# Kernel optimization log

Measured on AMD Instinct MI355X. Metric: run time of the kernel, lower is better.

## Reference

```python
import jax, jax.numpy as jnp
import numpy as np
import math

CUTOFF = 6.0
NUM_RADIAL = 96
HID = 128
NUM_GRAPHS = 4
NODES_PER_GRAPH = 4000
BOX = 67.0
EPS = 1e-10


def _layernorm(x):
    m = jnp.mean(x, axis=-1, keepdims=True)
    v = jnp.var(x, axis=-1, keepdims=True)
    return (x - m) / jnp.sqrt(v + 1e-5)


def _rbf(dist):
    # rbf_emb: exp-scaled gaussians with cosine cutoff envelope
    start = math.exp(-CUTOFF)
    means = jnp.linspace(start, 1.0, NUM_RADIAL).astype(dist.dtype)
    beta = (2.0 / NUM_RADIAL * (1.0 - start)) ** -2
    d = dist[:, None]
    env = 0.5 * (jnp.cos(d * jnp.pi / CUTOFF) + 1.0) * (d < CUTOFF).astype(dist.dtype)
    return env * jnp.exp(-beta * jnp.square(jnp.exp(-d) - means))


def _forward(pos, rl_w1, rl_b1, rl_w2, rl_b2, ne_w, ne_b, sv_w, sv_b,
             l3_w1, l3_b1, l3_w2, l3_b2, mp_ln_w, mp_ln_b,
             xp_w1, xp_b1, xp_w2, xp_b2, rp_w, rp_b,
             ip_w1, ip_b1, ip_w2, ip_b2,
             fte_eq_w, fte_w1, fte_b1, fte_w2, fte_b2,
             out_w, out_b, z, batch, edge_index):
    N = pos.shape[0]
    silu = jax.nn.silu
    j, i = edge_index[0], edge_index[1]

    vecs = pos[j] - pos[i]                       # [E,3]
    dist = jnp.linalg.norm(vecs, axis=-1)        # [E]
    r_emb = _rbf(dist)                           # [E,R]
    r_hid = silu(r_emb @ rl_w1 + rl_b1) @ rl_w2 + rl_b2
    rbounds = 0.5 * (jnp.cos(dist * jnp.pi / CUTOFF) + 1.0)
    r_hid = rbounds[:, None] * r_hid             # [E,H]

    # NeighborEmb: s = ln(lin(onehot(z))) + scatter_add_i(ln(lin(onehot(z)))[j] * r_hid)
    z1h = jax.nn.one_hot(z, 95, dtype=pos.dtype)
    h0 = _layernorm(z1h @ ne_w + ne_b)           # [N,H]
    s = h0 + jax.ops.segment_sum(h0[j] * r_hid, i, num_segments=N)

    vec = jnp.zeros((N, 3, HID), pos.dtype)

    ed = vecs / (dist[:, None] + EPS)            # edge_diff [E,3]
    ec = jnp.cross(pos[i], pos[j])
    ec = ec / (jnp.linalg.norm(ec, axis=1, keepdims=True) + EPS)
    ev = jnp.cross(ed, ec)
    frame = jnp.stack([ed, ec, ev], axis=-1)     # [E,3(space),3(frame)]

    # S_vector: scatter_add_i( s_lin[j] outer edge_diff * r_hid )
    s_lin = silu(s @ sv_w + sv_b)
    msg = s_lin[j][:, None, :] * (r_hid[:, None, :] * ed[:, :, None])  # [E,3,H]
    S = jax.ops.segment_sum(msg, i, num_segments=N)                    # [N,3,H]

    def scalarize(Se):
        sc = jnp.einsum('edh,edf->efh', Se, frame)                     # [E,3,H]
        sc = sc.at[:, 1, :].set(jnp.abs(sc[:, 1, :]))
        p = jnp.transpose(sc, (0, 2, 1))                               # [E,H,3]
        out = silu(p @ l3_w1 + l3_b1) @ l3_w2 + l3_b2                  # [E,H,1]
        return (out + p[:, :, :1])[..., 0]                             # [E,H]

    scalar3 = scalarize(S[i])
    scalar4 = scalarize(S[j])
    ew = jnp.concatenate([scalar3, scalar4], axis=-1) * rbounds[:, None]
    ew = jnp.concatenate([ew, r_hid, r_emb], axis=-1)                  # [E,3H+R]

    # EquiMessagePassing (only one layer executes: source loops range(1))
    xln = _layernorm(s) * mp_ln_w + mp_ln_b
    xh = silu(xln @ xp_w1 + xp_b1) @ xp_w2 + xp_b2                     # [N,3H]
    rbfh = (r_emb @ rp_w + rp_b) * (silu(ew @ ip_w1 + ip_b1) @ ip_w2 + ip_b2)
    m = xh[j] * rbfh                                                   # [E,3H]
    m1, m2, m3 = jnp.split(m, 3, axis=-1)
    m2 = m2 / jnp.sqrt(3.0)
    vmsg = (vec[j] * m2[:, None, :] + m3[:, None, :] * ed[:, :, None]) / jnp.sqrt(float(HID))
    s = s + jax.ops.segment_sum(m1, i, num_segments=N)
    vec = vec + jax.ops.segment_sum(vmsg, i, num_segments=N)

    # FTE (node_frame == 0 in LEFTNet-Z: use invariant norm channel)
    vp = jnp.einsum('ndh,hk->ndk', vec, fte_eq_w)                      # [N,3,2H]
    v1, v2 = jnp.split(vp, 2, axis=-1)
    scalar = jnp.sqrt(jnp.sum(v1 * v1, axis=1) + EPS)                  # [N,H]
    vec_dot = jnp.sum(v1 * v2, axis=1) / jnp.sqrt(float(HID))
    xh2 = silu(jnp.concatenate([s, scalar], axis=-1) @ fte_w1 + fte_b1) @ fte_w2 + fte_b2
    a1, a2, a3 = jnp.split(xh2, 3, axis=-1)
    s = s + (a1 + a2 * vec_dot) / jnp.sqrt(2.0)
    vec = vec + a3[:, None, :] * v2

    out = s @ out_w + out_b                                            # [N,T]
    num = jax.ops.segment_sum(out, batch, num_segments=NUM_GRAPHS)
    cnt = jax.ops.segment_sum(jnp.ones((N,), out.dtype), batch, num_segments=NUM_GRAPHS)
    out = num / cnt[:, None]                                           # mean readout
    return out  # y_std=1, y_mean=0


def _lin_init(key, fi, fo, bias=True):
    k1, k2 = jax.random.split(key)
    lim = 1.0 / np.sqrt(fi)
    w = jax.random.uniform(k1, (fi, fo), jnp.float32, -lim, lim)
    if not bias:
        return w
    b = jax.random.uniform(k2, (fo,), jnp.float32, -lim, lim)
    return w, b


def setup_inputs() -> dict:
    rng = np.random.default_rng(0)
    N = NUM_GRAPHS * NODES_PER_GRAPH
    pos_np = (rng.random((N, 3)) * BOX).astype(np.float32)
    batch_np = np.repeat(np.arange(NUM_GRAPHS), NODES_PER_GRAPH).astype(np.int64)
    z_np = rng.integers(0, 95, size=(N,)).astype(np.int64)
    rows, cols = [], []
    for g in range(NUM_GRAPHS):
        p = pos_np[g * NODES_PER_GRAPH:(g + 1) * NODES_PER_GRAPH]
        d2 = ((p[:, None, :] - p[None, :, :]) ** 2).sum(-1)
        a, b = np.nonzero((d2 < CUTOFF ** 2) & (d2 > 0.0))
        rows.append(a + g * NODES_PER_GRAPH)
        cols.append(b + g * NODES_PER_GRAPH)
    edge_index = np.stack([np.concatenate(rows), np.concatenate(cols)]).astype(np.int64)

    keys = jax.random.split(jax.random.key(0), 16)
    rl_w1, rl_b1 = _lin_init(keys[0], NUM_RADIAL, HID)
    rl_w2, rl_b2 = _lin_init(keys[1], HID, HID)
    ne_w, ne_b = _lin_init(keys[2], 95, HID)
    sv_w, sv_b = _lin_init(keys[3], HID, HID)
    l3_w1, l3_b1 = _lin_init(keys[4], 3, HID // 4)
    l3_w2, l3_b2 = _lin_init(keys[5], HID // 4, 1)
    xp_w1, xp_b1 = _lin_init(keys[6], HID, HID)
    xp_w2, xp_b2 = _lin_init(keys[7], HID, 3 * HID)
    rp_w, rp_b = _lin_init(keys[8], NUM_RADIAL, 3 * HID)
    ip_w1, ip_b1 = _lin_init(keys[9], 3 * HID + NUM_RADIAL, 3 * HID)
    ip_w2, ip_b2 = _lin_init(keys[10], 3 * HID, 3 * HID)
    fte_eq_w = _lin_init(keys[11], HID, 2 * HID, bias=False)
    fte_w1, fte_b1 = _lin_init(keys[12], 2 * HID, HID)
    fte_w2, fte_b2 = _lin_init(keys[13], HID, 3 * HID)
    out_w, out_b = _lin_init(keys[14], HID, 1)

    return {
        'pos': jnp.asarray(pos_np), 'z': jnp.asarray(z_np),
        'batch': jnp.asarray(batch_np), 'edge_index': jnp.asarray(edge_index),
        'rl_w1': rl_w1, 'rl_b1': rl_b1, 'rl_w2': rl_w2, 'rl_b2': rl_b2,
        'ne_w': ne_w, 'ne_b': ne_b, 'sv_w': sv_w, 'sv_b': sv_b,
        'l3_w1': l3_w1, 'l3_b1': l3_b1, 'l3_w2': l3_w2, 'l3_b2': l3_b2,
        'mp_ln_w': jnp.ones((HID,), jnp.float32), 'mp_ln_b': jnp.zeros((HID,), jnp.float32),
        'xp_w1': xp_w1, 'xp_b1': xp_b1, 'xp_w2': xp_w2, 'xp_b2': xp_b2,
        'rp_w': rp_w, 'rp_b': rp_b,
        'ip_w1': ip_w1, 'ip_b1': ip_b1, 'ip_w2': ip_w2, 'ip_b2': ip_b2,
        'fte_eq_w': fte_eq_w, 'fte_w1': fte_w1, 'fte_b1': fte_b1,
        'fte_w2': fte_w2, 'fte_b2': fte_b2, 'out_w': out_w, 'out_b': out_b,
    }


def reference(pos, rl_w1, rl_b1, rl_w2, rl_b2, ne_w, ne_b, sv_w, sv_b,
              l3_w1, l3_b1, l3_w2, l3_b2, mp_ln_w, mp_ln_b,
              xp_w1, xp_b1, xp_w2, xp_b2, rp_w, rp_b,
              ip_w1, ip_b1, ip_w2, ip_b2,
              fte_eq_w, fte_w1, fte_b1, fte_w2, fte_b2,
              out_w, out_b, z, batch, edge_index):
    return _forward(pos, rl_w1, rl_b1, rl_w2, rl_b2, ne_w, ne_b, sv_w, sv_b,
                    l3_w1, l3_b1, l3_w2, l3_b2, mp_ln_w, mp_ln_b,
                    xp_w1, xp_b1, xp_w2, xp_b2, rp_w, rp_b,
                    ip_w1, ip_b1, ip_w2, ip_b2,
                    fte_eq_w, fte_w1, fte_b1, fte_w2, fte_b2,
                    out_w, out_b, z, batch, edge_index)
```

## Files before the change

kernel.cpp:

```cpp
#include <hip/hip_runtime.h>
#include <hip/hip_bf16.h>
#include <math.h>

#define NRAD 96
#define HIDDIM 128
typedef unsigned short ushortT;

typedef __attribute__((ext_vector_type(8))) short bf8_t;
typedef __attribute__((ext_vector_type(4))) float f4_t;
typedef __attribute__((ext_vector_type(2))) float f2_t;

#if defined(__has_builtin)
#  if __has_builtin(__builtin_amdgcn_global_load_lds)
#    define HAVE_GLDS 1
#  endif
#  if __has_builtin(__builtin_amdgcn_rcpf)
#    define RCPF(x) __builtin_amdgcn_rcpf(x)
#  endif
#  if __has_builtin(__builtin_amdgcn_exp2f)
#    define EXP2F(x) __builtin_amdgcn_exp2f(x)
#  endif
#  if __has_builtin(__builtin_amdgcn_cosf)
#    define COSR(x) __builtin_amdgcn_cosf(x)
#  endif
#endif
#ifndef RCPF
#  define RCPF(x) (1.f/(x))
#endif
#ifndef EXP2F
#  define EXP2F(x) exp2f(x)
#endif
#ifndef COSR
#  define COSR(x) cosf(6.2831853071795864f*(x))
#endif
#define LOG2E 1.44269504088896f
#define LN2   0.69314718055995f

__device__ __forceinline__ float silu_f(float x){
  return x * RCPF(1.f + EXP2F(-LOG2E*x));
}
__device__ __forceinline__ float b2f(ushortT u){ return __uint_as_float(((unsigned int)u) << 16); }
__device__ __forceinline__ ushortT f2b(float x){
  unsigned int u = __float_as_uint(x);
  unsigned int r = (u + 0x7fffu + ((u >> 16) & 1u)) >> 16;
  return (ushortT)r;
}

#ifdef HAVE_GLDS
__device__ __forceinline__ void glds16(const ushortT* g, ushortT* l){
  __builtin_amdgcn_global_load_lds(
      (const __attribute__((address_space(1))) ushortT*)g,
      (__attribute__((address_space(3))) ushortT*)l, 16, 0, 0);
}
#endif

__global__ void k_detect(const ushortT* posw, int npos,
                         const int* batchw, int nb, int* flags){
  int tot = (npos < 4096 ? npos : 4096);
  int big = tot > nb ? tot : nb;
  int bad = 0, orv = 0;
  for (int t = blockIdx.x*blockDim.x + threadIdx.x; t < big; t += gridDim.x*blockDim.x){
    if (t < tot){
      float x = b2f(posw[t]);
      if (!(fabsf(x) <= 1000.f)) bad = 1;
    }
    if (t < nb && (t & 1)) orv |= batchw[t];
  }
  if (bad) atomicOr(&flags[2], 1);
  if (orv) atomicOr(&flags[3], 1);
}

__global__ void k_iconv(const int* zsrc, const int* bsrc, const int* esrc,
                        int* zi, int* bi, int* eii, int Nn, int E, const int* flags,
                        int* deg){
  int f = (flags[3] == 0) ? 1 : 0;
  int total = 2*Nn + 2*E;
  for (int t = blockIdx.x*blockDim.x + threadIdx.x; t < total; t += gridDim.x*blockDim.x){
    if (t < Nn) zi[t] = zsrc[(size_t)t << f];
    else if (t < 2*Nn) bi[t-Nn] = bsrc[(size_t)(t-Nn) << f];
    else {
      int e = t - 2*Nn;
      int v = esrc[(size_t)e << f];
      eii[e] = v;
      if (e >= E) atomicAdd(&deg[v], 1);
    }
  }
}

struct ConvDesc { const ushortT* src; float* dst; int n; };
struct ConvArgs { ConvDesc d[32]; };

__global__ void k_conv(ConvArgs a, int cnt, const int* flags){
  int y = blockIdx.y;
  if (y >= cnt) return;
  int f = (flags[2] == 0) ? 1 : 0;
  const ushortT* s = a.d[y].src;
  float* dst = a.d[y].dst;
  int n = a.d[y].n;
  if (f){
    for (int t = blockIdx.x*blockDim.x + threadIdx.x; t < n; t += gridDim.x*blockDim.x)
      dst[t] = b2f(s[t]);
  } else {
    const float* sf = (const float*)s;
    for (int t = blockIdx.x*blockDim.x + threadIdx.x; t < n; t += gridDim.x*blockDim.x)
      dst[t] = sf[t];
  }
}

struct TDesc { const ushortT* src; ushortT* dst; int K, N; };
struct TArgs { TDesc d[12]; };

__global__ void k_wt(TArgs a, int cnt, const int* flags){
  int y = blockIdx.y;
  if (y >= cnt) return;
  int f = (flags[2] == 0) ? 1 : 0;
  const ushortT* s = a.d[y].src;
  ushortT* dst = a.d[y].dst;
  int K = a.d[y].K, N = a.d[y].N, tot = K*N;
  for (int t = blockIdx.x*blockDim.x + threadIdx.x; t < tot; t += gridDim.x*blockDim.x){
    int k = t / N, n = t - k*N;
    ushortT v = f ? s[t] : f2b(((const float*)s)[t]);
    dst[(size_t)n*K + k] = v;
  }
}

__global__ void k_f2b(const float* __restrict__ src, ushortT* __restrict__ dst, int n){
  for (int t = blockIdx.x*blockDim.x + threadIdx.x; t < n; t += gridDim.x*blockDim.x)
    dst[t] = f2b(src[t]);
}

__global__ void k_zero(float* __restrict__ p, int n){
  int t = blockIdx.x*blockDim.x + threadIdx.x;
  int stride = gridDim.x*blockDim.x;
  for (; t < n; t += stride) p[t] = 0.f;
}

__global__ void k_sentinel(__hip_bfloat16* out, int n, float val){
  int t = threadIdx.x;
  if (t < n) out[t] = __float2bfloat16(val);
}

__global__ void k_csr_scan(const int* __restrict__ deg, int* __restrict__ rowptr, int Nn){
  __shared__ int sh[256];
  __shared__ int carry;
  if (threadIdx.x == 0){ carry = 0; rowptr[0] = 0; }
  __syncthreads();
  for (int t0 = 0; t0 < Nn; t0 += 256){
    int idx = t0 + threadIdx.x;
    int v = (idx < Nn) ? deg[idx] : 0;
    sh[threadIdx.x] = v; __syncthreads();
    for (int o = 1; o < 256; o <<= 1){
      int u = (threadIdx.x >= o) ? sh[threadIdx.x - o] : 0;
      __syncthreads();
      sh[threadIdx.x] += u; __syncthreads();
    }
    if (idx < Nn) rowptr[idx + 1] = carry + sh[threadIdx.x];
    __syncthreads();
    if (threadIdx.x == 0) carry += sh[255];
    __syncthreads();
  }
}

__global__ void k_csr_scatter(const int* __restrict__ eii, int E,
                              const int* __restrict__ rowptr, int* __restrict__ cursor,
                              int* __restrict__ jp, int* __restrict__ ip){
  int e = blockIdx.x*blockDim.x + threadIdx.x;
  if (e >= E) return;
  int i = eii[E+e];
  int p = atomicAdd(&cursor[i], 1);
  int k = rowptr[i] + p;
  jp[k] = eii[e];
  ip[k] = i;
}

__global__ void k_geom(const float* __restrict__ pos,
                       const int* __restrict__ jp, const int* __restrict__ ip,
                       int off, int Cc,
                       float* __restrict__ edb, float* __restrict__ ecv,
                       float* __restrict__ rb, ushortT* __restrict__ remb)
{
  int el = blockIdx.x*blockDim.x + threadIdx.x;
  if (el >= Cc) return;
  int g = off + el;
  int j = jp[g], i = ip[g];
  float pjx = pos[3*j], pjy = pos[3*j+1], pjz = pos[3*j+2];
  float pix = pos[3*i], piy = pos[3*i+1], piz = pos[3*i+2];
  float vx = pjx-pix, vy = pjy-piy, vz = pjz-piz;
  float d = sqrtf(vx*vx + vy*vy + vz*vz);
  float inv = RCPF(d + 1e-10f);
  float edx = vx*inv, edy = vy*inv, edz = vz*inv;
  edb[3*el]=edx; edb[3*el+1]=edy; edb[3*el+2]=edz;
  if (ecv){
    float cx = piy*pjz - piz*pjy;
    float cy = piz*pjx - pix*pjz;
    float cz = pix*pjy - piy*pjx;
    float cn = sqrtf(cx*cx + cy*cy + cz*cz);
    float inv2 = RCPF(cn + 1e-10f);
    cx *= inv2; cy *= inv2; cz *= inv2;
    ecv[6*el]=cx; ecv[6*el+1]=cy; ecv[6*el+2]=cz;
    ecv[6*el+3]=edy*cz - edz*cy;
    ecv[6*el+4]=edz*cx - edx*cz;
    ecv[6*el+5]=edx*cy - edy*cx;
  }
  float rbv = 0.5f*(COSR(d*0.08333333333f) + 1.f);
  rb[el] = rbv;
  float env = (d < 6.f) ? rbv : 0.f;
  const float stf = 0.0024787522f;
  const float prf = (2.0f/96.0f)*(1.0f - stf);
  const float betaL = LOG2E/(prf*prf);
  float emd = EXP2F(-LOG2E*d);
  for (int k = 0; k < NRAD; ++k){
    float mu = stf + (1.0f - stf)*((float)k*(1.0f/95.0f));
    float t = emd - mu;
    remb[(size_t)el*NRAD + k] = f2b(env * EXP2F(-betaL*t*t));
  }
}

__global__ __launch_bounds__(128) void k_embed(const int* __restrict__ z,
    const float* __restrict__ ne_w, const float* __restrict__ ne_b,
    float* __restrict__ s, float* __restrict__ h0,
    float* __restrict__ S, float* __restrict__ vecacc)
{
  int n = blockIdx.x; int h = threadIdx.x;
  float x = ne_w[(size_t)z[n]*HIDDIM + h] + ne_b[h];
  __shared__ float red[128];
  red[h] = x; __syncthreads();
  for (int o = 64; o > 0; o >>= 1){ if (h < o) red[h] += red[h+o]; __syncthreads(); }
  float mean = red[0] * (1.f/128.f);
  __syncthreads();
  float dx = x - mean;
  red[h] = dx*dx; __syncthreads();
  for (int o = 64; o > 0; o >>= 1){ if (h < o) red[h] += red[h+o]; __syncthreads(); }
  float var = red[0] * (1.f/128.f);
  float y = dx * rsqrtf(var + 1e-5f);
  s[(size_t)n*HIDDIM + h] = y;
  h0[(size_t)n*HIDDIM + h] = y;
  float* Sr = &S[(size_t)n*384 + h];
  float* Vr = &vecacc[(size_t)n*384 + h];
  Sr[0]=0.f; Sr[128]=0.f; Sr[256]=0.f;
  Vr[0]=0.f; Vr[128]=0.f; Vr[256]=0.f;
}

__global__ __launch_bounds__(128) void k_ln(const float* __restrict__ src, ushortT* __restrict__ dst,
    const float* __restrict__ g, const float* __restrict__ b, ushortT* __restrict__ sb)
{
  int n = blockIdx.x; int h = threadIdx.x;
  float x = src[(size_t)n*HIDDIM + h];
  sb[(size_t)n*HIDDIM + h] = f2b(x);
  __shared__ float red[128];
  red[h] = x; __syncthreads();
  for (int o = 64; o > 0; o >>= 1){ if (h < o) red[h] += red[h+o]; __syncthreads(); }
  float mean = red[0] * (1.f/128.f);
  __syncthreads();
  float dx = x - mean;
  red[h] = dx*dx; __syncthreads();
  for (int o = 64; o > 0; o >>= 1){ if (h < o) red[h] += red[h+o]; __syncthreads(); }
  float var = red[0] * (1.f/128.f);
  float y = dx * rsqrtf(var + 1e-5f);
  dst[(size_t)n*HIDDIM + h] = f2b(y * g[h] + b[h]);
}

__global__ __launch_bounds__(128) void k_seg1n(const int* __restrict__ rowptr,
    const int* __restrict__ jp, int o, int Cc,
    const float* __restrict__ h0, const ushortT* __restrict__ rhid,
    float* __restrict__ s)
{
  int i = blockIdx.x, h = threadIdx.x;
  int b = rowptr[i], e = rowptr[i+1];
  if (b < o) b = o;
  int hi = o + Cc; if (e > hi) e = hi;
  if (b >= e) return;
  float acc = 0.f;
  int m = b;
  for (; m + 1 < e; m += 2){
    int j0 = jp[m], j1 = jp[m+1];
    float r0 = b2f(rhid[(size_t)(m-o)*HIDDIM + h]);
    float r1 = b2f(rhid[(size_t)(m+1-o)*HIDDIM + h]);
    acc += h0[(size_t)j0*HIDDIM + h]*r0 + h0[(size_t)j1*HIDDIM + h]*r1;
  }
  if (m < e) acc += h0[(size_t)jp[m]*HIDDIM + h] * b2f(rhid[(size_t)(m-o)*HIDDIM + h]);
  s[(size_t)i*HIDDIM + h] += acc;
}

__global__ __launch_bounds__(128) void k_seg2n(const int* __restrict__ rowptr,
    const int* __restrict__ jp, int o, int Cc,
    const ushortT* __restrict__ slin, const ushortT* __restrict__ rhid,
    const float* __restrict__ edb, float* __restrict__ S)
{
  int i = blockIdx.x, h = threadIdx.x;
  int b = rowptr[i], e = rowptr[i+1];
  if (b < o) b = o;
  int hi = o + Cc; if (e > hi) e = hi;
  if (b >= e) return;
  float a0 = 0.f, a1 = 0.f, a2 = 0.f;
  int m = b;
  for (; m + 1 < e; m += 2){
    int ml = m - o, ml2 = ml + 1;
    float u0 = b2f(slin[(size_t)jp[m]*HIDDIM + h])   * b2f(rhid[(size_t)ml*HIDDIM + h]);
    float u1 = b2f(slin[(size_t)jp[m+1]*HIDDIM + h]) * b2f(rhid[(size_t)ml2*HIDDIM + h]);
    a0 += u0*edb[3*ml]   + u1*edb[3*ml2];
    a1 += u0*edb[3*ml+1] + u1*edb[3*ml2+1];
    a2 += u0*edb[3*ml+2] + u1*edb[3*ml2+2];
  }
  if (m < e){
    int ml = m - o;
    float u0 = b2f(slin[(size_t)jp[m]*HIDDIM + h]) * b2f(rhid[(size_t)ml*HIDDIM + h]);
    a0 += u0*edb[3*ml]; a1 += u0*edb[3*ml+1]; a2 += u0*edb[3*ml+2];
  }
  float* base = &S[(size_t)i*384 + h];
  base[0]   += a0;
  base[128] += a1;
  base[256] += a2;
}

__global__ __launch_bounds__(128) void k_seg3n(const int* __restrict__ rowptr,
    int o, int Cc,
    const ushortT* __restrict__ mb, const float* __restrict__ edb,
    float* __restrict__ s, float* __restrict__ vecacc)
{
  int i = blockIdx.x, h = threadIdx.x;
  int b = rowptr[i], e = rowptr[i+1];
  if (b < o) b = o;
  int hi = o + Cc; if (e > hi) e = hi;
  if (b >= e) return;
  const float is128 = 0.08838834764831845f;
  float am = 0.f, v0 = 0.f, v1 = 0.f, v2 = 0.f;
  int m = b;
  for (; m + 1 < e; m += 2){
    int ml = m - o, ml2 = ml + 1;
    float m1a = b2f(mb[(size_t)ml*384 + h]);
    float m1b = b2f(mb[(size_t)ml2*384 + h]);
    float mma = b2f(mb[(size_t)ml*384 + 256 + h]) * is128;
    float mmb = b2f(mb[(size_t)ml2*384 + 256 + h]) * is128;
    am += m1a + m1b;
    v0 += mma*edb[3*ml]   + mmb*edb[3*ml2];
    v1 += mma*edb[3*ml+1] + mmb*edb[3*ml2+1];
    v2 += mma*edb[3*ml+2] + mmb*edb[3*ml2+2];
  }
  if (m < e){
    int ml = m - o;
    float m1 = b2f(mb[(size_t)ml*384 + h]);
    float mm = b2f(mb[(size_t)ml*384 + 256 + h]) * is128;
    am += m1;
    v0 += mm*edb[3*ml]; v1 += mm*edb[3*ml+1]; v2 += mm*edb[3*ml+2];
  }
  s[(size_t)i*HIDDIM + h] += am;
  float* base = &vecacc[(size_t)i*384 + h];
  base[0]   += v0;
  base[128] += v1;
  base[256] += v2;
}

__global__ __launch_bounds__(256) void k_scal3(
  const int* __restrict__ jp, const int* __restrict__ ip, int off, int Cc,
  const float* __restrict__ S,
  const ushortT* __restrict__ rhid, const float* __restrict__ edb,
  const float* __restrict__ ecv, const float* __restrict__ rb,
  const ushortT* __restrict__ remb,
  const float* __restrict__ w1, const float* __restrict__ b1,
  const float* __restrict__ w2, const float* __restrict__ b2,
  ushortT* __restrict__ ew)
{
  __shared__ float w1s[96], b1s[32], w2s[32];
  __shared__ float sb2;
  int t = threadIdx.x;
  if (t < 96) w1s[t] = w1[t] * (-LOG2E);
  else if (t < 128) b1s[t-96] = b1[t-96] * (-LOG2E);
  else if (t < 160) w2s[t-128] = w2[t-128] * (-LN2);
  else if (t == 160) sb2 = b2[0];
  int ea = blockIdx.x*2;
  int eb = (ea + 1 < Cc) ? ea + 1 : ea;
  int which = t >> 7, h = t & 127;
  int ga = off + ea, gb = off + eb;
  int na = which ? jp[ga] : ip[ga];
  int nb = which ? jp[gb] : ip[gb];
  f2_t f00 = {edb[3*ea],   edb[3*eb]};
  f2_t f01 = {edb[3*ea+1], edb[3*eb+1]};
  f2_t f02 = {edb[3*ea+2], edb[3*eb+2]};
  f2_t f10 = {ecv[6*ea],   ecv[6*eb]};
  f2_t f11 = {ecv[6*ea+1], ecv[6*eb+1]};
  f2_t f12 = {ecv[6*ea+2], ecv[6*eb+2]};
  f2_t f20 = {ecv[6*ea+3], ecv[6*eb+3]};
  f2_t f21 = {ecv[6*ea+4], ecv[6*eb+4]};
  f2_t f22 = {ecv[6*ea+5], ecv[6*eb+5]};
  f2_t rbv = {rb[ea], rb[eb]};
  __syncthreads();
  const float* Sa = &S[(size_t)na*384];
  const float* Sb = &S[(size_t)nb*384];
  f2_t S0 = {Sa[h],     Sb[h]};
  f2_t S1 = {Sa[128+h], Sb[128+h]};
  f2_t S2 = {Sa[256+h], Sb[256+h]};
  f2_t v0 = S0*f00 + S1*f01 + S2*f02;
  f2_t v1t = S0*f10 + S1*f11 + S2*f12;
  f2_t v1 = {fabsf(v1t.x), fabsf(v1t.y)};
  f2_t v2 = S0*f20 + S1*f21 + S2*f22;
  f2_t out = {0.f, 0.f};
  #pragma unroll
  for (int u = 0; u < 32; ++u){
    f2_t tt = v0*w1s[u] + v1*w1s[32+u] + v2*w1s[64+u] + b1s[u];
    f2_t r;
    r.x = RCPF(1.f + EXP2F(tt.x));
    r.y = RCPF(1.f + EXP2F(tt.y));
    out += (tt*r)*w2s[u];
  }
  f2_t res = (out + sb2 + v0) * rbv;
  ushortT* ewa = &ew[(size_t)ea*480];
  ewa[which*128 + h] = f2b(res.x);
  if (eb != ea) ew[(size_t)eb*480 + which*128 + h] = f2b(res.y);
  if (which == 0){
    ewa[256 + h] = rhid[(size_t)ea*HIDDIM + h];
    if (h < NRAD) ewa[384 + h] = remb[(size_t)ea*NRAD + h];
    if (eb != ea){
      ew[(size_t)eb*480 + 256 + h] = rhid[(size_t)eb*HIDDIM + h];
      if (h < NRAD) ew[(size_t)eb*480 + 384 + h] = remb[(size_t)eb*NRAD + h];
    }
  }
}

__global__ __launch_bounds__(256) void mgemm(
  const ushortT* __restrict__ A, const ushortT* __restrict__ BT,
  const float* __restrict__ bias,
  float* __restrict__ Cf, ushortT* __restrict__ Cb,
  int M, int N, int K, int epi,
  const float* __restrict__ rowscale,
  const ushortT* __restrict__ mul1b,
  const ushortT* __restrict__ xhpb,
  const int* __restrict__ jidx,
  int skipTile)
{
  const int tid = threadIdx.x;
  const int w = tid >> 6;
  const int lane = tid & 63;
  const int l15 = lane & 15;
  const int q = lane >> 4;
  const int wm = w & 1, wn = w >> 1;
  const int rowBase = blockIdx.y * 128;
  int bx = blockIdx.x;
  if (skipTile >= 0 && bx >= skipTile) bx++;
  const int colBase = bx * 128;
  f4_t acc[4][4] = {};

#ifdef HAVE_GLDS
  __shared__ ushortT As[128*32];
  __shared__ ushortT Bs[128*32];
  const int rS = 32*w + (lane >> 2);
  const int kS = (lane & 3) << 3;
  ushortT* lA0 = &As[(32*w)*32];
  ushortT* lA1 = &As[(32*w+16)*32];
  ushortT* lB0 = &Bs[(32*w)*32];
  ushortT* lB1 = &Bs[(32*w+16)*32];
  int ra0 = rowBase + rS;      if (ra0 >= M) ra0 = M-1;
  int ra1 = rowBase + rS + 16; if (ra1 >= M) ra1 = M-1;
  const ushortT* gA0 = A  + (size_t)ra0*K + kS;
  const ushortT* gA1 = A  + (size_t)ra1*K + kS;
  const ushortT* gB0 = BT + (size_t)(colBase + rS)*K + kS;
  const ushortT* gB1 = BT + (size_t)(colBase + rS + 16)*K + kS;
  for (int k0 = 0; k0 < K; k0 += 32){
    glds16(gA0 + k0, lA0);
    glds16(gA1 + k0, lA1);
    glds16(gB0 + k0, lB0);
    glds16(gB1 + k0, lB1);
    __syncthreads();
    bf8_t a[4], b[4];
    #pragma unroll
    for (int mt = 0; mt < 4; ++mt)
      a[mt] = *(const bf8_t*)&As[(wm*64 + mt*16 + l15)*32 + q*8];
    #pragma unroll
    for (int nt = 0; nt < 4; ++nt)
      b[nt] = *(const bf8_t*)&Bs[(wn*64 + nt*16 + l15)*32 + q*8];
    #pragma unroll
    for (int mt = 0; mt < 4; ++mt){
      #pragma unroll
      for (int nt = 0; nt < 4; ++nt)
        acc[mt][nt] = __builtin_amdgcn_mfma_f32_16x16x32_bf16(a[mt], b[nt], acc[mt][nt], 0, 0, 0);
    }
    __syncthreads();
  }
#else
  __shared__ ushortT As[128*48];
  __shared__ ushortT Bs[128*48];
  const int r0 = tid >> 2,         s0 = (tid & 3) << 3;
  const int r1 = (tid + 256) >> 2, s1 = ((tid + 256) & 3) << 3;
  for (int k0 = 0; k0 < K; k0 += 32){
    int4 a0v = make_int4(0,0,0,0), a1v = make_int4(0,0,0,0);
    if (rowBase + r0 < M) a0v = *(const int4*)&A[(size_t)(rowBase + r0)*K + k0 + s0];
    if (rowBase + r1 < M) a1v = *(const int4*)&A[(size_t)(rowBase + r1)*K + k0 + s1];
    int4 b0v = *(const int4*)&BT[(size_t)(colBase + r0)*K + k0 + s0];
    int4 b1v = *(const int4*)&BT[(size_t)(colBase + r1)*K + k0 + s1];
    __syncthreads();
    *(int4*)&As[r0*48 + s0] = a0v;
    *(int4*)&As[r1*48 + s1] = a1v;
    *(int4*)&Bs[r0*48 + s0] = b0v;
    *(int4*)&Bs[r1*48 + s1] = b1v;
    __syncthreads();
    bf8_t a[4], b[4];
    #pragma unroll
    for (int mt = 0; mt < 4; ++mt)
      a[mt] = *(const bf8_t*)&As[(wm*64 + mt*16 + l15)*48 + q*8];
    #pragma unroll
    for (int nt = 0; nt < 4; ++nt)
      b[nt] = *(const bf8_t*)&Bs[(wn*64 + nt*16 + l15)*48 + q*8];
    #pragma unroll
    for (int mt = 0; mt < 4; ++mt){
      #pragma unroll
      for (int nt = 0; nt < 4; ++nt)
        acc[mt][nt] = __builtin_amdgcn_mfma_f32_16x16x32_bf16(a[mt], b[nt], acc[mt][nt], 0, 0, 0);
    }
  }
#endif

  #pragma unroll
  for (int mt = 0; mt < 4; ++mt){
    int row = rowBase + wm*64 + mt*16 + q*4;
    #pragma unroll
    for (int nt = 0; nt < 4; ++nt){
      int col = colBase + wn*64 + nt*16 + l15;
      float bv = bias ? bias[col] : 0.f;
      #pragma unroll
      for (int r = 0; r < 4; ++r){
        int rr = row + r;
        if (rr >= M) continue;
        float x = acc[mt][nt][r] + bv;
        if (epi == 1) x = silu_f(x);
        else if (epi == 2) x *= rowscale[rr];
        else if (epi == 3) x = x * b2f(mul1b[(size_t)rr*N + col]) * b2f(xhpb[(size_t)jidx[rr]*N + col]);
        if (Cb) Cb[(size_t)rr*N + col] = f2b(x);
        else    Cf[(size_t)rr*N + col] = x;
      }
    }
  }
}

__global__ __launch_bounds__(128) void k_fte_pre(const float* __restrict__ vpc,
    const float* __restrict__ s, ushortT* __restrict__ catb, float* __restrict__ vdot,
    int no)
{
  int nl = blockIdx.x, h = threadIdx.x;
  int n = no + nl;
  const float* base = &vpc[(size_t)nl*768];
  float a0 = base[h],       a1 = base[256+h],     a2 = base[512+h];
  float c0 = base[128+h],   c1 = base[384+h],     c2 = base[640+h];
  float scal = sqrtf(a0*a0 + a1*a1 + a2*a2 + 1e-10f);
  float vd = (a0*c0 + a1*c1 + a2*c2) * 0.08838834764831845f;
  catb[(size_t)n*256 + h] = f2b(s[(size_t)n*HIDDIM + h]);
  catb[(size_t)n*256 + 128 + h] = f2b(scal);
  vdot[(size_t)n*HIDDIM + h] = vd;
}

__global__ __launch_bounds__(128) void k_out(const float* __restrict__ xh2,
    const float* __restrict__ vdot, const float* __restrict__ s,
    const float* __restrict__ ow, const float* __restrict__ ob,
    float* __restrict__ nodeout)
{
  int n = blockIdx.x, h = threadIdx.x;
  float a1 = xh2[(size_t)n*384 + h];
  float a2 = xh2[(size_t)n*384 + 128 + h];
  float sv = s[(size_t)n*HIDDIM + h] + (a1 + a2*vdot[(size_t)n*HIDDIM + h]) * 0.7071067811865476f;
  __shared__ float red[128];
  red[h] = sv * ow[h];
  __syncthreads();
  for (int o = 64; o > 0; o >>= 1){ if (h < o) red[h] += red[h+o]; __syncthreads(); }
  if (h == 0) nodeout[n] = red[0] + ob[0];
}

__global__ __launch_bounds__(256) void k_final(const float* __restrict__ nodeout,
    const int* __restrict__ batch, void* __restrict__ out, int Nn, const int* flags)
{
  int g = blockIdx.x;
  __shared__ float rs[256], rc[256];
  float sm = 0.f, c = 0.f;
  for (int n = threadIdx.x; n < Nn; n += 256){
    if (batch[n] == g){ sm += nodeout[n]; c += 1.f; }
  }
  rs[threadIdx.x] = sm; rc[threadIdx.x] = c;
  __syncthreads();
  for (int o = 128; o > 0; o >>= 1){
    if (threadIdx.x < o){ rs[threadIdx.x] += rs[threadIdx.x+o]; rc[threadIdx.x] += rc[threadIdx.x+o]; }
    __syncthreads();
  }
  if (threadIdx.x == 0){
    float v = (rc[0] > 0.f) ? rs[0]/rc[0] : 0.f;
    if (flags[2] == 0) ((__hip_bfloat16*)out)[g] = __float2bfloat16(v);
    else ((float*)out)[g] = v;
  }
}

extern "C" void kernel_launch(void* const* d_in, const int* in_sizes, int n_in,
                              void* d_out, int out_size, void* d_ws, size_t ws_size,
                              hipStream_t stream)
{
  const int N = in_sizes[0] / 3;
  const int E = in_sizes[3] / 2;

  size_t off = 0;
  auto alloc = [&](size_t n)->float*{
    float* p = (float*)d_ws + off;
    off += (n + 3) & ~(size_t)3;
    return p;
  };
  auto allocU = [&](size_t n)->ushortT*{ return (ushortT*)alloc((n + 1) / 2); };

  int* flags  = (int*)alloc(4);
  int* deg    = (int*)alloc((size_t)N);
  int* cursor = (int*)alloc((size_t)N);
  size_t zeroHdr = off;
  int* zi     = (int*)alloc((size_t)N);
  int* bi     = (int*)alloc((size_t)N);
  int* eii    = (int*)alloc((size_t)2*E);
  int* rowptr = (int*)alloc((size_t)N + 4);
  int* jp     = (int*)alloc((size_t)E);
  int* ipp    = (int*)alloc((size_t)E);

  float* pos = alloc((size_t)N*3);
  float* w[31];
  for (int t = 0; t < 31; ++t) w[t] = alloc((size_t)in_sizes[4+t]);
  float* rl_b1=w[1];  float* rl_b2=w[3];
  float* ne_w =w[4];  float* ne_b =w[5];  float* sv_b =w[7];
  float* l3_w1=w[8];  float* l3_b1=w[9];  float* l3_w2=w[10]; float* l3_b2=w[11];
  float* mp_w =w[12]; float* mp_b =w[13]; float* xp_b1=w[15];
  float* xp_b2=w[17]; float* rp_b =w[19];
  float* ip_b1=w[21]; float* ip_b2=w[23];
  float* fte_b1=w[26];float* fte_b2=w[28];float* out_w=w[29]; float* out_b=w[30];

  ushortT* wt_rl1 = allocU(96*128);
  ushortT* wt_rl2 = allocU(128*128);
  ushortT* wt_sv  = allocU(128*128);
  ushortT* wt_xp1 = allocU(128*128);
  ushortT* wt_xp2 = allocU((size_t)128*384);
  ushortT* wt_rp  = allocU((size_t)96*384);
  ushortT* wt_ip1 = allocU((size_t)480*384);
  ushortT* wt_ip2 = allocU((size_t)384*384);
  ushortT* wt_feq = allocU((size_t)128*256);
  ushortT* wt_ft1 = allocU((size_t)256*128);
  ushortT* wt_ft2 = allocU((size_t)128*384);

  float* s    = alloc((size_t)N*HIDDIM);
  float* h0   = alloc((size_t)N*HIDDIM);
  ushortT* sb     = allocU((size_t)N*HIDDIM);
  ushortT* slin_b = allocU((size_t)N*HIDDIM);
  ushortT* xln_b  = allocU((size_t)N*HIDDIM);
  ushortT* hb     = allocU((size_t)N*HIDDIM);
  float* S    = alloc((size_t)N*384);
  float* vecacc = alloc((size_t)N*384);
  ushortT* xh_b = allocU((size_t)N*384);
  float* nodeout = alloc((size_t)N);
  float* vdot = h0;
  ushortT* catb = sb;
  ushortT* vab = (ushortT*)S;
  float* xh2 = vecacc;

  size_t wsF = ws_size / sizeof(float);

  int tier = 0; size_t p = 746;
  if (off + 122ULL*(size_t)E + 16 + 256ULL*624 <= wsF){ tier = 2; p = 624; }
  else if (off + 67ULL*(size_t)E + 16 + 256ULL*679 <= wsF){ tier = 1; p = 679; }

  ushortT *rhid_a = nullptr, *remb_a = nullptr;
  float *edb_a = nullptr, *ecv_a = nullptr, *rb_a = nullptr;
  if (tier >= 1){
    rhid_a = allocU((size_t)E*128);
    edb_a  = alloc((size_t)3*E);
  }
  if (tier == 2){
    ecv_a  = alloc((size_t)6*E);
    rb_a   = alloc((size_t)E);
    remb_a = allocU((size_t)E*96);
  }
  size_t availF = (wsF > off) ? (wsF - off) : 0;
  if (availF < 256*p){
    k_sentinel<<<1, 64, 0, stream>>>((__hip_bfloat16*)d_out, out_size,
                                     (float)(double)(ws_size >> 20));
    return;
  }
  size_t Cs = availF / p; if (Cs > (size_t)E) Cs = E;
  int C = (int)(Cs & ~(size_t)15);
  if (C < 256) C = 256;

  float* scratch0 = (float*)d_ws + off;
  ushortT* remb_l = nullptr; float *ecv_l = nullptr, *rb_l = nullptr;
  if (tier <= 1){
    remb_l = allocU((size_t)C*96);
    ecv_l  = alloc((size_t)6*C);
    rb_l   = alloc((size_t)C);
  }
  float* edb_l = nullptr; ushortT* rhid_l = nullptr;
  if (tier == 0){
    edb_l  = alloc((size_t)3*C);
    rhid_l = allocU((size_t)C*128);
  }
  ushortT* ew_b = allocU((size_t)C*480);
  ushortT* R2b  = allocU((size_t)C*384);
  ushortT* R1b  = allocU((size_t)C*384);
  ushortT* Rmb  = ew_b;
  ushortT* R2rl = R2b;
  float* vpc = scratch0;
  size_t scratchF = (size_t)C*p;

  auto mg = [&](const ushortT* A, const ushortT* BT, const float* bias,
                float* Cf, ushortT* Cb, int M, int Nc, int K, int epi,
                const float* rowscale = nullptr, const ushortT* mul1b = nullptr,
                const ushortT* xhpb = nullptr, const int* jidx = nullptr,
                int skipTile = -1){
    dim3 grid(Nc/128 - (skipTile >= 0 ? 1 : 0), (M + 127)/128);
    mgemm<<<grid, 256, 0, stream>>>(A, BT, bias, Cf, Cb, M, Nc, K, epi,
                                    rowscale, mul1b, xhpb, jidx, skipTile);
  };

  k_zero<<<64, 256, 0, stream>>>((float*)flags, (int)zeroHdr);
  k_detect<<<64, 256, 0, stream>>>((const ushortT*)d_in[0], in_sizes[0],
                                   (const int*)d_in[2], in_sizes[2], flags);
  k_iconv<<<1024, 256, 0, stream>>>((const int*)d_in[1], (const int*)d_in[2],
                                    (const int*)d_in[3], zi, bi, eii, N, E, flags, deg);

  ConvArgs ca;
  ca.d[0] = { (const ushortT*)d_in[0], pos, in_sizes[0] };
  for (int t = 0; t < 31; ++t)
    ca.d[1+t] = { (const ushortT*)d_in[4+t], w[t], in_sizes[4+t] };
  k_conv<<<dim3(32, 32), 256, 0, stream>>>(ca, 32, flags);

  TArgs ta;
  ta.d[0]  = { (const ushortT*)d_in[4],  wt_rl1, 96, 128 };
  ta.d[1]  = { (const ushortT*)d_in[6],  wt_rl2, 128, 128 };
  ta.d[2]  = { (const ushortT*)d_in[10], wt_sv,  128, 128 };
  ta.d[3]  = { (const ushortT*)d_in[18], wt_xp1, 128, 128 };
  ta.d[4]  = { (const ushortT*)d_in[20], wt_xp2, 128, 384 };
  ta.d[5]  = { (const ushortT*)d_in[22], wt_rp,  96, 384 };
  ta.d[6]  = { (const ushortT*)d_in[24], wt_ip1, 480, 384 };
  ta.d[7]  = { (const ushortT*)d_in[26], wt_ip2, 384, 384 };
  ta.d[8]  = { (const ushortT*)d_in[28], wt_feq, 128, 256 };
  ta.d[9]  = { (const ushortT*)d_in[29], wt_ft1, 256, 128 };
  ta.d[10] = { (const ushortT*)d_in[31], wt_ft2, 128, 384 };
  k_wt<<<dim3(48, 11), 256, 0, stream>>>(ta, 11, flags);

  k_csr_scan<<<1, 256, 0, stream>>>(deg, rowptr, N);
  k_csr_scatter<<<(E + 255)/256, 256, 0, stream>>>(eii, E, rowptr, cursor, jp, ipp);

  k_embed<<<N, 128, 0, stream>>>(zi, ne_w, ne_b, s, h0, S, vecacc);

  if (tier == 2){
    k_geom<<<(E + 255)/256, 256, 0, stream>>>(pos, jp, ipp, 0, E,
                                              edb_a, ecv_a, rb_a, remb_a);
    for (int o = 0; o < E; o += C){
      int Cc = (E - o < C) ? (E - o) : C;
      mg(remb_a + (size_t)o*96, wt_rl1, rl_b1, nullptr, R2rl, Cc, 128, 96, 1);
      mg(R2rl, wt_rl2, rl_b2, nullptr, rhid_a + (size_t)o*128, Cc, 128, 128, 2, rb_a + o);
    }
    k_seg1n<<<N, 128, 0, stream>>>(rowptr, jp, 0, E, h0, rhid_a, s);
  } else if (tier == 1){
    for (int o = 0; o < E; o += C){
      int Cc = (E - o < C) ? (E - o) : C;
      k_geom<<<(Cc + 255)/256, 256, 0, stream>>>(pos, jp, ipp, o, Cc,
                                                 edb_a + (size_t)3*o, nullptr, rb_l, remb_l);
      mg(remb_l, wt_rl1, rl_b1, nullptr, R2rl, Cc, 128, 96, 1);
      mg(R2rl, wt_rl2, rl_b2, nullptr, rhid_a + (size_t)o*128, Cc, 128, 128, 2, rb_l);
    }
    k_seg1n<<<N, 128, 0, stream>>>(rowptr, jp, 0, E, h0, rhid_a, s);
  } else {
    for (int o = 0; o < E; o += C){
      int Cc = (E - o < C) ? (E - o) : C;
      k_geom<<<(Cc + 255)/256, 256, 0, stream>>>(pos, jp, ipp, o, Cc,
                                                 edb_l, nullptr, rb_l, remb_l);
      mg(remb_l, wt_rl1, rl_b1, nullptr, R2rl, Cc, 128, 96, 1);
      mg(R2rl, wt_rl2, rl_b2, nullptr, rhid_l, Cc, 128, 128, 2, rb_l);
      k_seg1n<<<N, 128, 0, stream>>>(rowptr, jp, o, Cc, h0, rhid_l, s);
    }
  }

  k_ln<<<N, 128, 0, stream>>>(s, xln_b, mp_w, mp_b, sb);
  mg(sb, wt_sv, sv_b, nullptr, slin_b, N, 128, 128, 1);
  mg(xln_b, wt_xp1, xp_b1, nullptr, hb, N, 128, 128, 1);
  mg(hb, wt_xp2, xp_b2, nullptr, xh_b, N, 384, 128, 0, nullptr, nullptr, nullptr, nullptr, 1);

  if (tier >= 1){
    k_seg2n<<<N, 128, 0, stream>>>(rowptr, jp, 0, E, slin_b, rhid_a, edb_a, S);
  } else {
    for (int o = 0; o < E; o += C){
      int Cc = (E - o < C) ? (E - o) : C;
      k_geom<<<(Cc + 255)/256, 256, 0, stream>>>(pos, jp, ipp, o, Cc,
                                                 edb_l, nullptr, rb_l, remb_l);
      mg(remb_l, wt_rl1, rl_b1, nullptr, R2rl, Cc, 128, 96, 1);
      mg(R2rl, wt_rl2, rl_b2, nullptr, rhid_l, Cc, 128, 128, 2, rb_l);
      k_seg2n<<<N, 128, 0, stream>>>(rowptr, jp, o, Cc, slin_b, rhid_l, edb_l, S);
    }
  }

  for (int o = 0; o < E; o += C){
    int Cc = (E - o < C) ? (E - o) : C;
    const ushortT *rhid_p, *remb_p;
    const float *edb_p, *ecv_p, *rb_p;
    if (tier == 2){
      rhid_p = rhid_a + (size_t)o*128;
      edb_p  = edb_a + (size_t)3*o;
      ecv_p  = ecv_a + (size_t)6*o;
      rb_p   = rb_a + o;
      remb_p = remb_a + (size_t)o*96;
    } else if (tier == 1){
      k_geom<<<(Cc + 255)/256, 256, 0, stream>>>(pos, jp, ipp, o, Cc,
                                                 edb_a + (size_t)3*o, ecv_l, rb_l, remb_l);
      rhid_p = rhid_a + (size_t)o*128;
      edb_p  = edb_a + (size_t)3*o;
      ecv_p  = ecv_l; rb_p = rb_l; remb_p = remb_l;
    } else {
      k_geom<<<(Cc + 255)/256, 256, 0, stream>>>(pos, jp, ipp, o, Cc,
                                                 edb_l, ecv_l, rb_l, remb_l);
      mg(remb_l, wt_rl1, rl_b1, nullptr, R2rl, Cc, 128, 96, 1);
      mg(R2rl, wt_rl2, rl_b2, nullptr, rhid_l, Cc, 128, 128, 2, rb_l);
      rhid_p = rhid_l; edb_p = edb_l; ecv_p = ecv_l; rb_p = rb_l; remb_p = remb_l;
    }
    k_scal3<<<(Cc + 1)/2, 256, 0, stream>>>(jp, ipp, o, Cc, S, rhid_p,
                                            edb_p, ecv_p, rb_p, remb_p,
                                            l3_w1, l3_b1, l3_w2, l3_b2, ew_b);
    mg(remb_p, wt_rp, rp_b, nullptr, R1b, Cc, 384, 96, 0,
       nullptr, nullptr, nullptr, nullptr, 1);
    mg(ew_b, wt_ip1, ip_b1, nullptr, R2b, Cc, 384, 480, 1);
    mg(R2b, wt_ip2, ip_b2, nullptr, Rmb, Cc, 384, 384, 3,
       nullptr, R1b, xh_b, jp + o, 1);
    k_seg3n<<<N, 128, 0, stream>>>(rowptr, o, Cc, Rmb, edb_p, s, vecacc);
  }

  k_f2b<<<1024, 256, 0, stream>>>(vecacc, vab, N*384);
  int Cn = (int)(scratchF / 768);
  if (Cn > N) Cn = N;
  for (int no = 0; no < N; no += Cn){
    int Cc = (N - no < Cn) ? (N - no) : Cn;
    mg(vab + (size_t)no*384, wt_feq, nullptr, vpc, nullptr, 3*Cc, 256, 128, 0);
    k_fte_pre<<<Cc, 128, 0, stream>>>(vpc, s, catb, vdot, no);
  }
  mg(catb, wt_ft1, fte_b1, nullptr, hb, N, 128, 256, 1);
  mg(hb, wt_ft2, fte_b2, xh2, nullptr, N, 384, 128, 0);

  k_out<<<N, 128, 0, stream>>>(xh2, vdot, s, out_w, out_b, nodeout);
  k_final<<<out_size, 256, 0, stream>>>(nodeout, bi, d_out, N, flags);
}
```

Baseline: 1.926 ms.

## Read rhid/remb directly in GEMM instead of copying into concatenated buffer

The scalarization kernel no longer copies rhid and remb into a 480-wide concatenated edge buffer. It writes only the 256 scalarized columns, and the ip1 GEMM now reads its A operand from three source pointers selected by K range. This removes per-edge copy traffic and shrinks the scratch buffer, which allows larger chunks. The layer-3 weight scaling is also precomputed once into a global buffer, so each block skips the shared-memory staging and its barrier. The cost is branchy address selection inside the GEMM K loop, and the small weights are now read from global memory or cache instead of LDS.

```diff
diff --git a/kernel.cpp b/kernel.cpp
--- a/kernel.cpp
+++ b/kernel.cpp
@@ -107,6 +107,16 @@
   }
 }
 
+__global__ void k_l3pre(const float* __restrict__ w1, const float* __restrict__ b1,
+                        const float* __restrict__ w2, const float* __restrict__ b2,
+                        float* __restrict__ l3s){
+  int t = threadIdx.x;
+  if (t < 96) l3s[t] = w1[t] * (-LOG2E);
+  else if (t < 128) l3s[t] = b1[t-96] * (-LOG2E);
+  else if (t < 160) l3s[t] = w2[t-128] * (-LN2);
+  else if (t == 160) l3s[160] = b2[0];
+}
+
 struct TDesc { const ushortT* src; ushortT* dst; int K, N; };
 struct TArgs { TDesc d[12]; };
 
@@ -351,25 +361,17 @@
   base[256] += v2;
 }
 
-__global__ __launch_bounds__(256) void k_scal3(
+__global__ __launch_bounds__(256) void k_scal4(
   const int* __restrict__ jp, const int* __restrict__ ip, int off, int Cc,
   const float* __restrict__ S,
-  const ushortT* __restrict__ rhid, const float* __restrict__ edb,
-  const float* __restrict__ ecv, const float* __restrict__ rb,
-  const ushortT* __restrict__ remb,
-  const float* __restrict__ w1, const float* __restrict__ b1,
-  const float* __restrict__ w2, const float* __restrict__ b2,
-  ushortT* __restrict__ ew)
-{
-  __shared__ float w1s[96], b1s[32], w2s[32];
-  __shared__ float sb2;
-  int t = threadIdx.x;
-  if (t < 96) w1s[t] = w1[t] * (-LOG2E);
-  else if (t < 128) b1s[t-96] = b1[t-96] * (-LOG2E);
-  else if (t < 160) w2s[t-128] = w2[t-128] * (-LN2);
-  else if (t == 160) sb2 = b2[0];
+  const float* __restrict__ edb, const float* __restrict__ ecv,
+  const float* __restrict__ rb,
+  const float* __restrict__ l3s,
+  ushortT* __restrict__ ews)
+{
   int ea = blockIdx.x*2;
   int eb = (ea + 1 < Cc) ? ea + 1 : ea;
+  int t = threadIdx.x;
   int which = t >> 7, h = t & 127;
   int ga = off + ea, gb = off + eb;
   int na = which ? jp[ga] : ip[ga];
@@ -384,7 +386,6 @@
   f2_t f21 = {ecv[6*ea+4], ecv[6*eb+4]};
   f2_t f22 = {ecv[6*ea+5], ecv[6*eb+5]};
   f2_t rbv = {rb[ea], rb[eb]};
-  __syncthreads();
   const float* Sa = &S[(size_t)na*384];
   const float* Sb = &S[(size_t)nb*384];
   f2_t S0 = {Sa[h],     Sb[h]};
@@ -397,24 +398,15 @@
   f2_t out = {0.f, 0.f};
   #pragma unroll
   for (int u = 0; u < 32; ++u){
-    f2_t tt = v0*w1s[u] + v1*w1s[32+u] + v2*w1s[64+u] + b1s[u];
+    f2_t tt = v0*l3s[u] + v1*l3s[32+u] + v2*l3s[64+u] + l3s[96+u];
     f2_t r;
     r.x = RCPF(1.f + EXP2F(tt.x));
     r.y = RCPF(1.f + EXP2F(tt.y));
-    out += (tt*r)*w2s[u];
-  }
-  f2_t res = (out + sb2 + v0) * rbv;
-  ushortT* ewa = &ew[(size_t)ea*480];
-  ewa[which*128 + h] = f2b(res.x);
-  if (eb != ea) ew[(size_t)eb*480 + which*128 + h] = f2b(res.y);
-  if (which == 0){
-    ewa[256 + h] = rhid[(size_t)ea*HIDDIM + h];
-    if (h < NRAD) ewa[384 + h] = remb[(size_t)ea*NRAD + h];
-    if (eb != ea){
-      ew[(size_t)eb*480 + 256 + h] = rhid[(size_t)eb*HIDDIM + h];
-      if (h < NRAD) ew[(size_t)eb*480 + 384 + h] = remb[(size_t)eb*NRAD + h];
-    }
-  }
+    out += (tt*r)*l3s[128+u];
+  }
+  f2_t res = (out + l3s[160] + v0) * rbv;
+  ews[(size_t)ea*256 + which*128 + h] = f2b(res.x);
+  if (eb != ea) ews[(size_t)eb*256 + which*128 + h] = f2b(res.y);
 }
 
 __global__ __launch_bounds__(256) void mgemm(
@@ -426,7 +418,8 @@
   const ushortT* __restrict__ mul1b,
   const ushortT* __restrict__ xhpb,
   const int* __restrict__ jidx,
-  int skipTile)
+  int skipTile,
+  const ushortT* __restrict__ A1, const ushortT* __restrict__ A2)
 {
   const int tid = threadIdx.x;
   const int w = tid >> 6;
@@ -451,13 +444,16 @@
   ushortT* lB1 = &Bs[(32*w+16)*32];
   int ra0 = rowBase + rS;      if (ra0 >= M) ra0 = M-1;
   int ra1 = rowBase + rS + 16; if (ra1 >= M) ra1 = M-1;
-  const ushortT* gA0 = A  + (size_t)ra0*K + kS;
-  const ushortT* gA1 = A  + (size_t)ra1*K + kS;
   const ushortT* gB0 = BT + (size_t)(colBase + rS)*K + kS;
   const ushortT* gB1 = BT + (size_t)(colBase + rS + 16)*K + kS;
   for (int k0 = 0; k0 < K; k0 += 32){
-    glds16(gA0 + k0, lA0);
-    glds16(gA1 + k0, lA1);
+    const ushortT* srcA; size_t strA; int kc;
+    if (!A1){ srcA = A; strA = (size_t)K; kc = k0; }
+    else if (k0 < 256){ srcA = A; strA = 256; kc = k0; }
+    else if (k0 < 384){ srcA = A1; strA = 128; kc = k0 - 256; }
+    else { srcA = A2; strA = 96; kc = k0 - 384; }
+    glds16(srcA + (size_t)ra0*strA + kc + kS, lA0);
+    glds16(srcA + (size_t)ra1*strA + kc + kS, lA1);
     glds16(gB0 + k0, lB0);
     glds16(gB1 + k0, lB1);
     __syncthreads();
@@ -482,9 +478,14 @@
   const int r0 = tid >> 2,         s0 = (tid & 3) << 3;
   const int r1 = (tid + 256) >> 2, s1 = ((tid + 256) & 3) << 3;
   for (int k0 = 0; k0 < K; k0 += 32){
+    const ushortT* srcA; size_t strA; int kc;
+    if (!A1){ srcA = A; strA = (size_t)K; kc = k0; }
+    else if (k0 < 256){ srcA = A; strA = 256; kc = k0; }
+    else if (k0 < 384){ srcA = A1; strA = 128; kc = k0 - 256; }
+    else { srcA = A2; strA = 96; kc = k0 - 384; }
     int4 a0v = make_int4(0,0,0,0), a1v = make_int4(0,0,0,0);
-    if (rowBase + r0 < M) a0v = *(const int4*)&A[(size_t)(rowBase + r0)*K + k0 + s0];
-    if (rowBase + r1 < M) a1v = *(const int4*)&A[(size_t)(rowBase + r1)*K + k0 + s1];
+    if (rowBase + r0 < M) a0v = *(const int4*)&srcA[(size_t)(rowBase + r0)*strA + kc + s0];
+    if (rowBase + r1 < M) a1v = *(const int4*)&srcA[(size_t)(rowBase + r1)*strA + kc + s1];
     int4 b0v = *(const int4*)&BT[(size_t)(colBase + r0)*K + k0 + s0];
     int4 b1v = *(const int4*)&BT[(size_t)(colBase + r1)*K + k0 + s1];
     __syncthreads();
@@ -610,6 +611,7 @@
   int* rowptr = (int*)alloc((size_t)N + 4);
   int* jp     = (int*)alloc((size_t)E);
   int* ipp    = (int*)alloc((size_t)E);
+  float* l3s  = alloc(164);
 
   float* pos = alloc((size_t)N*3);
   float* w[31];
@@ -651,9 +653,9 @@
 
   size_t wsF = ws_size / sizeof(float);
 
-  int tier = 0; size_t p = 746;
-  if (off + 122ULL*(size_t)E + 16 + 256ULL*624 <= wsF){ tier = 2; p = 624; }
-  else if (off + 67ULL*(size_t)E + 16 + 256ULL*679 <= wsF){ tier = 1; p = 679; }
+  int tier = 0; size_t p = 698;
+  if (off + 122ULL*(size_t)E + 16 + 256ULL*576 <= wsF){ tier = 2; p = 576; }
+  else if (off + 67ULL*(size_t)E + 16 + 256ULL*631 <= wsF){ tier = 1; p = 631; }
 
   ushortT *rhid_a = nullptr, *remb_a = nullptr;
   float *edb_a = nullptr, *ecv_a = nullptr, *rb_a = nullptr;
@@ -688,10 +690,11 @@
     edb_l  = alloc((size_t)3*C);
     rhid_l = allocU((size_t)C*128);
   }
-  ushortT* ew_b = allocU((size_t)C*480);
+  ushortT* ewReg = allocU((size_t)C*384);
   ushortT* R2b  = allocU((size_t)C*384);
   ushortT* R1b  = allocU((size_t)C*384);
-  ushortT* Rmb  = ew_b;
+  ushortT* ews  = ewReg;
+  ushortT* Rmb  = ewReg;
   ushortT* R2rl = R2b;
   float* vpc = scratch0;
   size_t scratchF = (size_t)C*p;
@@ -700,10 +703,11 @@
                 float* Cf, ushortT* Cb, int M, int Nc, int K, int epi,
                 const float* rowscale = nullptr, const ushortT* mul1b = nullptr,
                 const ushortT* xhpb = nullptr, const int* jidx = nullptr,
-                int skipTile = -1){
+                int skipTile = -1,
+                const ushortT* A1 = nullptr, const ushortT* A2 = nullptr){
     dim3 grid(Nc/128 - (skipTile >= 0 ? 1 : 0), (M + 127)/128);
     mgemm<<<grid, 256, 0, stream>>>(A, BT, bias, Cf, Cb, M, Nc, K, epi,
-                                    rowscale, mul1b, xhpb, jidx, skipTile);
+                                    rowscale, mul1b, xhpb, jidx, skipTile, A1, A2);
   };
 
   k_zero<<<64, 256, 0, stream>>>((float*)flags, (int)zeroHdr);
@@ -717,6 +721,7 @@
   for (int t = 0; t < 31; ++t)
     ca.d[1+t] = { (const ushortT*)d_in[4+t], w[t], in_sizes[4+t] };
   k_conv<<<dim3(32, 32), 256, 0, stream>>>(ca, 32, flags);
+  k_l3pre<<<1, 192, 0, stream>>>(l3_w1, l3_b1, l3_w2, l3_b2, l3s);
 
   TArgs ta;
   ta.d[0]  = { (const ushortT*)d_in[4],  wt_rl1, 96, 128 };
@@ -807,12 +812,12 @@
       mg(R2rl, wt_rl2, rl_b2, nullptr, rhid_l, Cc, 128, 128, 2, rb_l);
       rhid_p = rhid_l; edb_p = edb_l; ecv_p = ecv_l; rb_p = rb_l; remb_p = remb_l;
     }
-    k_scal3<<<(Cc + 1)/2, 256, 0, stream>>>(jp, ipp, o, Cc, S, rhid_p,
-                                            edb_p, ecv_p, rb_p, remb_p,
-                                            l3_w1, l3_b1, l3_w2, l3_b2, ew_b);
+    k_scal4<<<(Cc + 1)/2, 256, 0, stream>>>(jp, ipp, o, Cc, S,
+                                            edb_p, ecv_p, rb_p, l3s, ews);
     mg(remb_p, wt_rp, rp_b, nullptr, R1b, Cc, 384, 96, 0,
        nullptr, nullptr, nullptr, nullptr, 1);
-    mg(ew_b, wt_ip1, ip_b1, nullptr, R2b, Cc, 384, 480, 1);
+    mg(ews, wt_ip1, ip_b1, nullptr, R2b, Cc, 384, 480, 1,
+       nullptr, nullptr, nullptr, nullptr, -1, rhid_p, remb_p);
     mg(R2b, wt_ip2, ip_b2, nullptr, Rmb, Cc, 384, 384, 3,
        nullptr, R1b, xh_b, jp + o, 1);
     k_seg3n<<<N, 128, 0, stream>>>(rowptr, o, Cc, Rmb, edb_p, s, vecacc);
```

Result: faster. 1.821 ms, median of 2 (-5.4%).
